# Optimization experiments

Hardware: AMD Instinct MI355X
Metric: run time of the kernel (lower is better)

The kernel has to match this reference:

```python
import jax, jax.numpy as jnp
import numpy as np

DT = 0.01  # init kwarg dt
M = 501    # microstructure feature length (hardcoded split [501, 501] in source)
H = 128    # hidden width


def _mlp(x, W1, b1, W2, b2):
    # Linear -> Softplus -> Linear
    return jax.nn.softplus(x @ W1 + b1) @ W2 + b2


def _linear_init(key, fan_in, fan_out):
    k1, k2 = jax.random.split(key)
    s = 1.0 / np.sqrt(fan_in)
    W = jax.random.uniform(k1, (fan_in, fan_out), minval=-s, maxval=s, dtype=jnp.float32)
    b = jax.random.uniform(k2, (fan_out,), minval=-s, maxval=s, dtype=jnp.float32)
    return W, b


def setup_inputs() -> dict:
    key = jax.random.key(0)
    ks = jax.random.split(key, 10)
    B, T = 32768, 512
    Ew1, Eb1 = _linear_init(ks[0], 2 * M, H)   # energy net: Linear(1002,128)
    Ew2, Eb2 = _linear_init(ks[1], H, 1)
    nw1, nb1 = _linear_init(ks[2], M, H)       # nu net: Linear(501,128)
    nw2, nb2 = _linear_init(ks[3], H, 1)
    bw1, bb1 = _linear_init(ks[4], 2 * M, H)   # beta net: Linear(1002,128)
    bw2, bb2 = _linear_init(ks[5], H, 1)
    e = jax.random.normal(ks[6], (B, T, 1), dtype=jnp.float32) * 0.01
    e_dot = jax.random.normal(ks[7], (B, T, 1), dtype=jnp.float32) * 0.01
    E = jax.random.uniform(ks[8], (B, M), dtype=jnp.float32)
    nu = jax.random.uniform(ks[9], (B, M), dtype=jnp.float32)
    return dict(e=e, e_dot=e_dot, E=E, nu=nu,
                Ew1=Ew1, Eb1=Eb1, Ew2=Ew2, Eb2=Eb2,
                nw1=nw1, nb1=nb1, nw2=nw2, nb2=nb2,
                bw1=bw1, bb1=bb1, bw2=bw2, bb2=bb2)


def reference(e, e_dot, E, nu,
              Ew1, Eb1, Ew2, Eb2,
              nw1, nb1, nw2, nb2,
              bw1, bb1, bw2, bb2):
    # microstructure encoder: m = concat(E, nu) -> [B, 1002]; constant over time,
    # so the three small MLPs are evaluated ONCE (the per-step autograd.grad of the
    # quadratic energy/dissipation potentials has closed form).
    m = jnp.concatenate((E, nu), axis=-1)
    Emod = jnp.exp(_mlp(m, Ew1, Eb1, Ew2, Eb2))                              # exp(E(m))    [B,1]
    nu_feat = m[:, M:]                                                        # second half of split
    nuv = jnp.exp(jnp.square(_mlp(nu_feat, nw1, nb1, nw2, nb2)) / 40000.0)    # exp(nu(.))   [B,1]
    beta = jnp.square(_mlp(m, bw1, bb1, bw2, bb2)) / 40000.0                  # beta(m)      [B,1]

    # Per-step closed-form derivatives of
    #   energy    = 1/2 exp(E(m)) u^2 + 1/2 (u - v)^2        (u = e_t, v = xi_t)
    #   potential = -1/2 exp(nu) p^2 + 1/2 sum(beta q^2)     (p = e_dot_t, q = -dE/dv = e_t - xi_t)
    #   s_eq = exp(E) u + (u - v);  s_neq = dPhi/dp = -exp(nu) p;  kinetics = dPhi/dq = beta q
    def step(xi, inputs):
        et, edt = inputs                     # [B,1] each
        q = et - xi
        stress_t = Emod * et + q + nuv * edt  # s_eq - s_neq
        xi_next = xi + DT * beta * q
        return xi_next, (stress_t, xi)

    xi0 = jnp.zeros_like(e[:, 0])            # [B,1]
    eT = jnp.moveaxis(e, 1, 0)               # [T,B,1]
    edT = jnp.moveaxis(e_dot, 1, 0)
    _, (stress, xi) = jax.lax.scan(step, xi0, (eT, edT))
    return jnp.moveaxis(stress, 0, 1), jnp.moveaxis(xi, 0, 1)  # [B,T,1] each
```

## Files before the change

### kernel.cpp

```cpp
#include <hip/hip_runtime.h>
#include <hip/hip_bf16.h>

#define M_ 501
#define T_ 512
#define DT_ 0.01f

typedef __attribute__((ext_vector_type(8))) __bf16 bf16x8;
typedef __attribute__((ext_vector_type(4))) float f32x4;

static __device__ __forceinline__ unsigned int pack2(float a, float b) {
    __hip_bfloat16 ha = __float2bfloat16(a);
    __hip_bfloat16 hb = __float2bfloat16(b);
    unsigned short ua = __builtin_bit_cast(unsigned short, ha);
    unsigned short ub = __builtin_bit_cast(unsigned short, hb);
    return (unsigned int)ua | ((unsigned int)ub << 16);
}

__global__ void build_w(const float* __restrict__ Ew1, const float* __restrict__ bw1,
                        const float* __restrict__ nw1, __hip_bfloat16* __restrict__ Wswz) {
    int idx = blockIdx.x * 256 + threadIdx.x;
    if (idx >= 32 * 24 * 64 * 8) return;
    int e  = idx & 7;
    int l  = (idx >> 3) & 63;
    int t  = idx >> 9;
    int nt = t % 24, k0 = t / 24;
    int k  = k0 * 32 + ((l >> 4) << 3) + e;
    int n  = nt * 16 + (l & 15);
    float v = 0.f;
    if (n < 128)      { if (k < 2*M_)             v = Ew1[k * 128 + n]; }
    else if (n < 256) { if (k < 2*M_)             v = bw1[k * 128 + (n - 128)]; }
    else              { if (k >= M_ && k < 2*M_)  v = nw1[(k - M_) * 128 + (n - 256)]; }
    Wswz[idx] = __float2bfloat16(v);
}

__global__ __launch_bounds__(512, 2) void mlp_gemm5(
    const float* __restrict__ E, const float* __restrict__ nu,
    const __hip_bfloat16* __restrict__ Wswz,
    const float* __restrict__ Eb1, const float* __restrict__ bb1, const float* __restrict__ nb1,
    const float* __restrict__ Ew2, const float* __restrict__ bw2, const float* __restrict__ nw2,
    const float* __restrict__ Eb2, const float* __restrict__ bb2, const float* __restrict__ nb2,
    float* __restrict__ Emod, float* __restrict__ nuv, float* __restrict__ beta, int B)
{
    const int tid = threadIdx.x;
    const int wid = tid >> 6, l = tid & 63;
    const int c = l & 15, g = l >> 4;
    const int brow = blockIdx.x * 64;

    __shared__ __align__(16) unsigned char sAraw[2][64 * 128];
    __shared__ float cb1[384], cw2[384];
    __shared__ float lds_s[3][64];

    if (tid < 384) {
        int n = tid;
        cb1[n] = (n < 128) ? Eb1[n] : (n < 256) ? bb1[n - 128] : nb1[n - 256];
        cw2[n] = (n < 128) ? Ew2[n] : (n < 256) ? bw2[n - 128] : nw2[n - 256];
    }
    if (tid < 192) ((float*)lds_s)[tid] = 0.f;

    f32x4 q0, q1, q2; int ofs;
    const int sr = tid >> 3, su = tid & 7;
    const size_t rb = (size_t)(brow + sr) * M_;
    auto stage_load = [&](int ch) {
        int cu = ch * 8 + su;
        bool slow = (cu == 62) | (cu >= 124);
        if (!slow) {
            const float* src = (cu < 62) ? E : nu;
            int off = (cu < 62) ? cu * 8 : cu * 8 - M_;
            size_t s = rb + (size_t)off;
            ofs = (int)(s & 3);
            const f32x4* p = (const f32x4*)(src + (s & ~(size_t)3));
            q0 = p[0]; q1 = p[1]; q2 = p[2];
        } else {
            int kb = cu * 8;
            auto ldx = [&](int k) -> float {
                return (k < M_) ? E[rb + k] : ((k < 2 * M_) ? nu[rb + k - M_] : 0.f);
            };
            q0 = (f32x4){ldx(kb+0), ldx(kb+1), ldx(kb+2), ldx(kb+3)};
            q1 = (f32x4){ldx(kb+4), ldx(kb+5), ldx(kb+6), ldx(kb+7)};
            q2 = (f32x4){0.f, 0.f, 0.f, 0.f};
            ofs = 0;
        }
    };
    auto stage_finish = [&](int nbuf) {
        asm volatile("" : "+v"(q0), "+v"(q1), "+v"(q2));
        float g0=q0[0], g1=q0[1], g2=q0[2], g3=q0[3],
              g4=q1[0], g5=q1[1], g6=q1[2], g7=q1[3],
              g8=q2[0], g9=q2[1], g10=q2[2];
        const bool o2 = (ofs & 2) != 0, o1 = (ofs & 1) != 0;
        float u0 = o2?g2:g0, u1 = o2?g3:g1, u2 = o2?g4:g2, u3 = o2?g5:g3,
              u4 = o2?g6:g4, u5 = o2?g7:g5, u6 = o2?g8:g6, u7 = o2?g9:g7,
              u8 = o2?g10:g8;
        float f0 = o1?u1:u0, f1 = o1?u2:u1, f2 = o1?u3:u2, f3 = o1?u4:u3,
              f4 = o1?u5:u4, f5 = o1?u6:u5, f6 = o1?u7:u6, f7 = o1?u8:u7;
        uint4 vv;
        vv.x = pack2(f0, f1); vv.y = pack2(f2, f3);
        vv.z = pack2(f4, f5); vv.w = pack2(f6, f7);
        unsigned bo = ((unsigned)sr << 7) + ((((unsigned)su) << 4) ^ (((unsigned)(sr & 7)) << 4));
        *(uint4*)(sAraw[nbuf] + bo) = vv;
    };

    const bf16x8* wbase = (const bf16x8*)Wswz;
    auto loadW3 = [&](bf16x8 (&w)[3], int kg) {
        #pragma unroll
        for (int nt = 0; nt < 3; ++nt)
            w[nt] = wbase[(size_t)(kg * 24 + wid * 3 + nt) * 64 + l];
    };

    f32x4 acc[4][3];
    #pragma unroll
    for (int mi = 0; mi < 4; mi++)
        #pragma unroll
        for (int nt = 0; nt < 3; nt++) acc[mi][nt] = (f32x4){0.f, 0.f, 0.f, 0.f};
    bf16x8 wa[3], wb[3], af[4];

    auto readAF = [&](int buf, int kk) {
        #pragma unroll
        for (int mi = 0; mi < 4; ++mi) {
            int row = c + mi * 16;
            unsigned bo = ((unsigned)row << 7) +
                ((((unsigned)kk << 6) + ((unsigned)g << 4)) ^ (((unsigned)(row & 7)) << 4));
            af[mi] = *(const bf16x8*)(sAraw[buf] + bo);
        }
    };
    auto M12 = [&](bf16x8 (&w)[3]) {
        #pragma unroll
        for (int nt = 0; nt < 3; ++nt)
            #pragma unroll
            for (int mi = 0; mi < 4; ++mi)
                acc[mi][nt] = __builtin_amdgcn_mfma_f32_16x16x32_bf16(w[nt], af[mi], acc[mi][nt], 0, 0, 0);
    };

    stage_load(0);
    stage_finish(0);
    __syncthreads();

    for (int ch = 0; ch < 16; ++ch) {
        const int buf = ch & 1;
        if (ch < 15) stage_load(ch + 1);
        const int kg = ch * 2;
        loadW3(wa, kg + 0);
        loadW3(wb, kg + 1);
        readAF(buf, 0); M12(wa);
        readAF(buf, 1); M12(wb);
        if (ch < 15) stage_finish(buf ^ 1);
        __syncthreads();
    }

    float bv[12], wv[12];
    #pragma unroll
    for (int nt = 0; nt < 3; ++nt)
        #pragma unroll
        for (int r = 0; r < 4; ++r) {
            int nidx = (wid * 3 + nt) * 16 + g * 4 + r;
            bv[nt * 4 + r] = cb1[nidx];
            wv[nt * 4 + r] = cw2[nidx];
        }
    const int m_first = (wid * 3) >> 3, m_last = (wid * 3 + 2) >> 3;

    #pragma unroll
    for (int mi = 0; mi < 4; ++mi) {
        float s0 = 0.f, s1 = 0.f, s2 = 0.f;
        #pragma unroll
        for (int nt = 0; nt < 3; ++nt) {
            float p = 0.f;
            #pragma unroll
            for (int r = 0; r < 4; ++r) {
                float x = acc[mi][nt][r] + bv[nt * 4 + r];
                float h = fmaxf(x, 0.f) + __logf(1.f + __expf(-fabsf(x)));
                p += h * wv[nt * 4 + r];
            }
            int m = (wid * 3 + nt) >> 3;
            if (m == 0) s0 += p; else if (m == 1) s1 += p; else s2 += p;
        }
        auto red = [&](float v, int m) {
            v += __shfl_xor(v, 16);
            v += __shfl_xor(v, 32);
            if (l < 16) atomicAdd(&lds_s[m][mi * 16 + l], v);
        };
        if (m_first == 0) red(s0, 0);
        if (m_first <= 1 && m_last >= 1) red(s1, 1);
        if (m_last == 2) red(s2, 2);
    }
    __syncthreads();

    if (tid < 64) {
        int b = brow + tid;
        float s0 = lds_s[0][tid], s1 = lds_s[1][tid], s2 = lds_s[2][tid];
        Emod[b] = __expf(s0 + Eb2[0]);
        float mb = s1 + bb2[0];
        beta[b]  = mb * mb * (1.f / 40000.f);
        float mn = s2 + nb2[0];
        nuv[b]   = __expf(mn * mn * (1.f / 40000.f));
    }
}

__global__ __launch_bounds__(256) void scan_k(
    const float* __restrict__ e, const float* __restrict__ ed,
    const float* __restrict__ Emod, const float* __restrict__ nuv, const float* __restrict__ beta,
    float* __restrict__ stress, float* __restrict__ xiout)
{
    int lane = threadIdx.x & 63;
    int b = blockIdx.x * 4 + (threadIdx.x >> 6);
    float Em = Emod[b], nv = nuv[b], bt = beta[b];
    float cc = DT_ * bt;
    float a  = 1.f - cc;

    size_t base = (size_t)b * T_ + (size_t)lane * 8;
    float4 e0 = *(const float4*)(e + base),  e1 = *(const float4*)(e + base + 4);
    float4 d0 = *(const float4*)(ed + base), d1 = *(const float4*)(ed + base + 4);
    float ev[8] = {e0.x, e0.y, e0.z, e0.w, e1.x, e1.y, e1.z, e1.w};
    float dv[8] = {d0.x, d0.y, d0.z, d0.w, d1.x, d1.y, d1.z, d1.w};

    float S = 0.f;
    #pragma unroll
    for (int j = 0; j < 8; j++) S = a * S + ev[j];
    float a2 = a * a, a4 = a2 * a2, A = a4 * a4;

    #pragma unroll
    for (int d = 1; d < 64; d <<= 1) {
        float Su = __shfl_up(S, d);
        float Au = __shfl_up(A, d);
        if (lane >= d) { S = Su * A + S; A = Au * A; }
    }
    float Sp = __shfl_up(S, 1);
    float xi = (lane == 0) ? 0.f : cc * Sp;

    float st[8], xo[8];
    #pragma unroll
    for (int j = 0; j < 8; j++) {
        xo[j] = xi;
        float qd = ev[j] - xi;
        st[j] = Em * ev[j] + qd + nv * dv[j];
        xi = xi + cc * qd;
    }
    *(float4*)(stress + base)     = (float4){st[0], st[1], st[2], st[3]};
    *(float4*)(stress + base + 4) = (float4){st[4], st[5], st[6], st[7]};
    *(float4*)(xiout + base)      = (float4){xo[0], xo[1], xo[2], xo[3]};
    *(float4*)(xiout + base + 4)  = (float4){xo[4], xo[5], xo[6], xo[7]};
}

extern "C" void kernel_launch(void* const* d_in, const int* in_sizes, int n_in,
                              void* d_out, int out_size, void* d_ws, size_t ws_size,
                              hipStream_t stream) {
    const float* e   = (const float*)d_in[0];
    const float* ed  = (const float*)d_in[1];
    const float* E   = (const float*)d_in[2];
    const float* nu  = (const float*)d_in[3];
    const float* Ew1 = (const float*)d_in[4];
    const float* Eb1 = (const float*)d_in[5];
    const float* Ew2 = (const float*)d_in[6];
    const float* Eb2 = (const float*)d_in[7];
    const float* nw1 = (const float*)d_in[8];
    const float* nb1 = (const float*)d_in[9];
    const float* nw2 = (const float*)d_in[10];
    const float* nb2 = (const float*)d_in[11];
    const float* bw1 = (const float*)d_in[12];
    const float* bb1 = (const float*)d_in[13];
    const float* bw2 = (const float*)d_in[14];
    const float* bb2 = (const float*)d_in[15];

    int B = in_sizes[2] / M_;

    char* ws = (char*)d_ws;
    __hip_bfloat16* Wswz = (__hip_bfloat16*)ws;
    float* Emod = (float*)(ws + (size_t)1024 * 384 * 2);
    float* nuv  = Emod + B;
    float* beta = nuv + B;

    build_w<<<(1024 * 384 + 255) / 256, 256, 0, stream>>>(Ew1, bw1, nw1, Wswz);
    mlp_gemm5<<<B / 64, 512, 0, stream>>>(E, nu, Wswz, Eb1, bb1, nb1,
                                          Ew2, bw2, nw2, Eb2, bb2, nb2,
                                          Emod, nuv, beta, B);
    float* stress = (float*)d_out;
    float* xiout  = stress + (size_t)B * T_;
    scan_k<<<B / 4, 256, 0, stream>>>(e, ed, Emod, nuv, beta, stress, xiout);
}
```

Baseline: 113.2 us.

## Fuse MLP GEMM and time scan into one kernel with pipelined weight loads

```diff
diff --git a/kernel.cpp b/kernel.cpp
--- a/kernel.cpp
+++ b/kernel.cpp
@@ -33,13 +33,14 @@
     Wswz[idx] = __float2bfloat16(v);
 }
 
-__global__ __launch_bounds__(512, 2) void mlp_gemm5(
+__global__ __launch_bounds__(512, 4) void fused_all(
     const float* __restrict__ E, const float* __restrict__ nu,
     const __hip_bfloat16* __restrict__ Wswz,
     const float* __restrict__ Eb1, const float* __restrict__ bb1, const float* __restrict__ nb1,
     const float* __restrict__ Ew2, const float* __restrict__ bw2, const float* __restrict__ nw2,
     const float* __restrict__ Eb2, const float* __restrict__ bb2, const float* __restrict__ nb2,
-    float* __restrict__ Emod, float* __restrict__ nuv, float* __restrict__ beta, int B)
+    const float* __restrict__ e, const float* __restrict__ ed,
+    float* __restrict__ stress, float* __restrict__ xiout, int B)
 {
     const int tid = threadIdx.x;
     const int wid = tid >> 6, l = tid & 63;
@@ -111,7 +112,7 @@
     for (int mi = 0; mi < 4; mi++)
         #pragma unroll
         for (int nt = 0; nt < 3; nt++) acc[mi][nt] = (f32x4){0.f, 0.f, 0.f, 0.f};
-    bf16x8 wa[3], wb[3], af[4];
+    bf16x8 wcur[3], wnxt[3], af[4];
 
     auto readAF = [&](int buf, int kk) {
         #pragma unroll
@@ -131,17 +132,18 @@
     };
 
     stage_load(0);
+    loadW3(wcur, 0);
     stage_finish(0);
     __syncthreads();
 
     for (int ch = 0; ch < 16; ++ch) {
         const int buf = ch & 1;
+        const int kg = ch * 2;
+        loadW3(wnxt, kg + 1);
         if (ch < 15) stage_load(ch + 1);
-        const int kg = ch * 2;
-        loadW3(wa, kg + 0);
-        loadW3(wb, kg + 1);
-        readAF(buf, 0); M12(wa);
-        readAF(buf, 1); M12(wb);
+        readAF(buf, 0); M12(wcur);
+        if (ch < 15) loadW3(wcur, kg + 2);
+        readAF(buf, 1); M12(wnxt);
         if (ch < 15) stage_finish(buf ^ 1);
         __syncthreads();
     }
@@ -184,59 +186,55 @@
     __syncthreads();
 
     if (tid < 64) {
-        int b = brow + tid;
         float s0 = lds_s[0][tid], s1 = lds_s[1][tid], s2 = lds_s[2][tid];
-        Emod[b] = __expf(s0 + Eb2[0]);
+        lds_s[0][tid] = __expf(s0 + Eb2[0]);
         float mb = s1 + bb2[0];
-        beta[b]  = mb * mb * (1.f / 40000.f);
+        lds_s[1][tid] = mb * mb * (1.f / 40000.f);
         float mn = s2 + nb2[0];
-        nuv[b]   = __expf(mn * mn * (1.f / 40000.f));
-    }
-}
-
-__global__ __launch_bounds__(256) void scan_k(
-    const float* __restrict__ e, const float* __restrict__ ed,
-    const float* __restrict__ Emod, const float* __restrict__ nuv, const float* __restrict__ beta,
-    float* __restrict__ stress, float* __restrict__ xiout)
-{
-    int lane = threadIdx.x & 63;
-    int b = blockIdx.x * 4 + (threadIdx.x >> 6);
-    float Em = Emod[b], nv = nuv[b], bt = beta[b];
-    float cc = DT_ * bt;
-    float a  = 1.f - cc;
-
-    size_t base = (size_t)b * T_ + (size_t)lane * 8;
-    float4 e0 = *(const float4*)(e + base),  e1 = *(const float4*)(e + base + 4);
-    float4 d0 = *(const float4*)(ed + base), d1 = *(const float4*)(ed + base + 4);
-    float ev[8] = {e0.x, e0.y, e0.z, e0.w, e1.x, e1.y, e1.z, e1.w};
-    float dv[8] = {d0.x, d0.y, d0.z, d0.w, d1.x, d1.y, d1.z, d1.w};
-
-    float S = 0.f;
-    #pragma unroll
-    for (int j = 0; j < 8; j++) S = a * S + ev[j];
-    float a2 = a * a, a4 = a2 * a2, A = a4 * a4;
-
-    #pragma unroll
-    for (int d = 1; d < 64; d <<= 1) {
-        float Su = __shfl_up(S, d);
-        float Au = __shfl_up(A, d);
-        if (lane >= d) { S = Su * A + S; A = Au * A; }
-    }
-    float Sp = __shfl_up(S, 1);
-    float xi = (lane == 0) ? 0.f : cc * Sp;
-
-    float st[8], xo[8];
-    #pragma unroll
-    for (int j = 0; j < 8; j++) {
-        xo[j] = xi;
-        float qd = ev[j] - xi;
-        st[j] = Em * ev[j] + qd + nv * dv[j];
-        xi = xi + cc * qd;
-    }
-    *(float4*)(stress + base)     = (float4){st[0], st[1], st[2], st[3]};
-    *(float4*)(stress + base + 4) = (float4){st[4], st[5], st[6], st[7]};
-    *(float4*)(xiout + base)      = (float4){xo[0], xo[1], xo[2], xo[3]};
-    *(float4*)(xiout + base + 4)  = (float4){xo[4], xo[5], xo[6], xo[7]};
+        lds_s[2][tid] = __expf(mn * mn * (1.f / 40000.f));
+    }
+    __syncthreads();
+
+    for (int i = 0; i < 8; ++i) {
+        const int rr = wid * 8 + i;
+        const int b = brow + rr;
+        float Em = lds_s[0][rr], bt = lds_s[1][rr], nv = lds_s[2][rr];
+        float cc = DT_ * bt;
+        float a  = 1.f - cc;
+
+        size_t base = (size_t)b * T_ + (size_t)l * 8;
+        float4 e0 = *(const float4*)(e + base),  e1 = *(const float4*)(e + base + 4);
+        float4 d0 = *(const float4*)(ed + base), d1 = *(const float4*)(ed + base + 4);
+        float ev[8] = {e0.x, e0.y, e0.z, e0.w, e1.x, e1.y, e1.z, e1.w};
+        float dv[8] = {d0.x, d0.y, d0.z, d0.w, d1.x, d1.y, d1.z, d1.w};
+
+        float S = 0.f;
+        #pragma unroll
+        for (int j = 0; j < 8; j++) S = a * S + ev[j];
+        float a2 = a * a, a4 = a2 * a2, A = a4 * a4;
+
+        #pragma unroll
+        for (int d = 1; d < 64; d <<= 1) {
+            float Su = __shfl_up(S, d);
+            float Au = __shfl_up(A, d);
+            if (l >= d) { S = Su * A + S; A = Au * A; }
+        }
+        float Sp = __shfl_up(S, 1);
+        float xi = (l == 0) ? 0.f : cc * Sp;
+
+        float st[8], xo[8];
+        #pragma unroll
+        for (int j = 0; j < 8; j++) {
+            xo[j] = xi;
+            float qd = ev[j] - xi;
+            st[j] = Em * ev[j] + qd + nv * dv[j];
+            xi = xi + cc * qd;
+        }
+        *(float4*)(stress + base)     = (float4){st[0], st[1], st[2], st[3]};
+        *(float4*)(stress + base + 4) = (float4){st[4], st[5], st[6], st[7]};
+        *(float4*)(xiout + base)      = (float4){xo[0], xo[1], xo[2], xo[3]};
+        *(float4*)(xiout + base + 4)  = (float4){xo[4], xo[5], xo[6], xo[7]};
+    }
 }
 
 extern "C" void kernel_launch(void* const* d_in, const int* in_sizes, int n_in,
@@ -263,15 +261,12 @@
 
     char* ws = (char*)d_ws;
     __hip_bfloat16* Wswz = (__hip_bfloat16*)ws;
-    float* Emod = (float*)(ws + (size_t)1024 * 384 * 2);
-    float* nuv  = Emod + B;
-    float* beta = nuv + B;
-
-    build_w<<<(1024 * 384 + 255) / 256, 256, 0, stream>>>(Ew1, bw1, nw1, Wswz);
-    mlp_gemm5<<<B / 64, 512, 0, stream>>>(E, nu, Wswz, Eb1, bb1, nb1,
-                                          Ew2, bw2, nw2, Eb2, bb2, nb2,
-                                          Emod, nuv, beta, B);
+
     float* stress = (float*)d_out;
     float* xiout  = stress + (size_t)B * T_;
-    scan_k<<<B / 4, 256, 0, stream>>>(e, ed, Emod, nuv, beta, stress, xiout);
-}
+
+    build_w<<<(1024 * 384 + 255) / 256, 256, 0, stream>>>(Ew1, bw1, nw1, Wswz);
+    fused_all<<<B / 64, 512, 0, stream>>>(E, nu, Wswz, Eb1, bb1, nb1,
+                                          Ew2, bw2, nw2, Eb2, bb2, nb2,
+                                          e, ed, stress, xiout, B);
+}
```

After: 110.9 us. -2.0%, faster.
